# Performance work log

Measured on AMD Instinct MI355X. Metric: run time of the kernel, lower is better.

Reference implementation:

```python
import jax, jax.numpy as jnp
import numpy as np

B, S, M = 1, 2048, 2048
H, HKV, D = 32, 8, 64
SW = 128
WAVELENGTH = 150000.0
SCALE = D ** (-0.25)
NEG = -1e9  # large negative for fp32 compute dtype


def setup_inputs() -> dict:
    key = jax.random.key(0)
    ks = jax.random.split(key, 8)
    return {
        "hidden_states": jax.random.normal(ks[0], (B, S, M), jnp.float32),
        "Wq": jax.random.normal(ks[1], (M, H, D), jnp.float32) * 0.02,
        "bq": jnp.zeros((H, D), jnp.float32),
        "Wk": jax.random.normal(ks[2], (M, HKV, D), jnp.float32) * 0.02,
        "bk": jnp.zeros((HKV, D), jnp.float32),
        "Wv": jax.random.normal(ks[3], (M, HKV, D), jnp.float32) * 0.02,
        "bv": jnp.zeros((HKV, D), jnp.float32),
        "Wo": jax.random.normal(ks[4], (H, D, M), jnp.float32) * 0.02,
        "bo": jnp.zeros((M,), jnp.float32),
        "sinks": jax.random.normal(ks[5], (H,), jnp.float32),
    }


def _cos_sin(seq_len, dtype):
    # yarn RoPE with scaling_factor=1.0 reduces to standard RoPE (mscale=1,
    # no frequency interpolation). half = D//2 frequencies.
    half = D // 2
    inv_freq = 1.0 / (WAVELENGTH ** (jnp.arange(half, dtype=jnp.float32) * 2.0 / D))
    t = jnp.arange(seq_len, dtype=jnp.float32)
    freqs = t[:, None] * inv_freq[None, :]  # [S, half]
    # broadcast shape [1, S, 1, half] to match [B, S, heads, half]
    return (jnp.cos(freqs)[None, :, None, :].astype(dtype),
            jnp.sin(freqs)[None, :, None, :].astype(dtype))


def _interleaved_rope(x, cos, sin):
    x_even = x[..., ::2]
    x_odd = x[..., 1::2]
    first = x_even * cos - x_odd * sin
    second = x_odd * cos + x_even * sin
    return jnp.stack([first, second], axis=-1).reshape(x.shape)


def reference(hidden_states, Wq, bq, Wk, bk, Wv, bv, Wo, bo, sinks):
    b, s, _ = hidden_states.shape
    groups = H // HKV

    q = jnp.einsum('bqm,muh->bquh', hidden_states, Wq) + bq  # [B,S,H,D]
    k = jnp.einsum('bkm,mvh->bkvh', hidden_states, Wk) + bk  # [B,S,HKV,D]
    v = jnp.einsum('bkm,mvh->bkvh', hidden_states, Wv) + bv

    cos, sin = _cos_sin(s, hidden_states.dtype)
    q = _interleaved_rope(q, cos, sin) * SCALE
    k = _interleaved_rope(k, cos, sin) * SCALE

    # GQA: repeat kv heads to match query heads
    k = jnp.repeat(k, groups, axis=2)  # [B,S,H,D]
    v = jnp.repeat(v, groups, axis=2)

    scores = jnp.einsum('bquh,bkuh->buqk', q, k)  # [B,H,S,S]

    pos = jnp.arange(s)
    sw_mask = jnp.abs(pos[:, None] - pos[None, :]) <= SW  # bidirectional window
    scores = jnp.where(sw_mask[None, None, :, :], scores, NEG)

    sink_logits = jnp.broadcast_to(sinks[None, :, None, None], (b, H, s, 1))
    combined = jnp.concatenate([scores, sink_logits], axis=-1)  # [B,H,S,S+1]
    probs = jax.nn.softmax(combined.astype(jnp.float32), axis=-1)
    attn = probs[..., :-1].astype(hidden_states.dtype)  # drop sink column

    out = jnp.einsum('buqk,bkuh->bquh', attn, v)  # [B,S,H,D]
    return jnp.einsum('bquh,uhm->bqm', out, Wo) + bo
```

## Files before the change

kernel.cpp:

```cpp
#include <hip/hip_runtime.h>
#include <hip/hip_bf16.h>
#include <stdint.h>

typedef unsigned short u16;
typedef unsigned int   u32;

#define S_LEN 2048
#define NQKV  3072
#define NH    32
#define NKV   8
#define SWIN  128
#define NEGV  (-1.0e9f)
#define SCALE_Q 0.35355339059327379f

typedef __attribute__((ext_vector_type(4)))  float  f32x4;
typedef __attribute__((ext_vector_type(16))) float  f32x16;
typedef __attribute__((ext_vector_type(8)))  __bf16 bf16x8;

__device__ __forceinline__ u16 f2bf(float x){
  u32 u = __float_as_uint(x);
  return (u16)((u + 0x7fffu + ((u >> 16) & 1u)) >> 16);
}
__device__ __forceinline__ u32 pk2(float a, float b){
  return (u32)f2bf(a) | ((u32)f2bf(b) << 16);
}
__device__ __forceinline__ f32x4 mfma16(bf16x8 a, bf16x8 b, f32x4 c){
  return __builtin_amdgcn_mfma_f32_16x16x32_bf16(a, b, c, 0, 0, 0);
}
__device__ __forceinline__ f32x16 mfma32(bf16x8 a, bf16x8 b, f32x16 c){
  return __builtin_amdgcn_mfma_f32_32x32x16_bf16(a, b, c, 0, 0, 0);
}

typedef __attribute__((address_space(1))) const unsigned int ga_u32;
typedef __attribute__((address_space(3))) unsigned int       ls_u32;
__device__ __forceinline__ void gl16(const void* g, void* l){
  __builtin_amdgcn_global_load_lds((ga_u32*)g, (ls_u32*)l, 16, 0, 0);
}

__global__ __launch_bounds__(256) void k_prep(const float* __restrict__ bq,
                                              const float* __restrict__ bk,
                                              const float* __restrict__ bv,
                                              float* __restrict__ ropetab,
                                              float* __restrict__ bias3){
  int id = blockIdx.x * 256 + threadIdx.x;
  int t = id >> 5, i = id & 31;
  float e = (i * 2.0f) / 64.0f;
  float base = (float)pow(150000.0, (double)e);
  float invf = 1.0f / base;
  float fr = (float)t * invf;
  ropetab[(size_t)id * 2 + 0] = cosf(fr);
  ropetab[(size_t)id * 2 + 1] = sinf(fr);
  if (id < NQKV){
    float b;
    if (id < 2048) b = bq[id];
    else if (id < 2560) b = bk[id - 2048];
    else b = bv[id - 2560];
    bias3[id] = b;
  }
}

__device__ __forceinline__ void packw_seg(const float* __restrict__ w,
                                          u16* __restrict__ oh,
                                          int N, int NTot, int nOff, int id){
  int p = id / N, n = id % N;
  u32 hw[4];
  #pragma unroll
  for (int j = 0; j < 4; ++j){
    float a = w[(size_t)(8 * p + 2 * j) * N + n];
    float b = w[(size_t)(8 * p + 2 * j + 1) * N + n];
    hw[j] = pk2(a, b);
  }
  size_t o = ((size_t)p * NTot + nOff + n) * 8;
  *(uint4*)(oh + o) = make_uint4(hw[0], hw[1], hw[2], hw[3]);
}
__global__ __launch_bounds__(256) void k_packall(const float* __restrict__ hid,
                                                 const float* __restrict__ Wq,
                                                 const float* __restrict__ Wk,
                                                 const float* __restrict__ Wv,
                                                 const float* __restrict__ Wo,
                                                 u16* __restrict__ Ah,
                                                 u16* __restrict__ Bh,
                                                 u16* __restrict__ Woh){
  int b = blockIdx.x;
  if (b < 2048){
    int id = b * 256 + threadIdx.x;
    int r = id >> 8, p = id & 255;
    const float4* src = (const float4*)(hid + (size_t)id * 8);
    float4 v0 = src[0], v1 = src[1];
    u32 hw[4];
    hw[0] = pk2(v0.x, v0.y); hw[1] = pk2(v0.z, v0.w);
    hw[2] = pk2(v1.x, v1.y); hw[3] = pk2(v1.z, v1.w);
    int psw = (p & ~7) | ((p & 7) ^ (r & 7));
    size_t o = ((size_t)r * 256 + psw) * 8;
    *(uint4*)(Ah + o) = make_uint4(hw[0], hw[1], hw[2], hw[3]);
  } else if (b < 4096){
    packw_seg(Wq, Bh, 2048, NQKV, 0,    (b - 2048) * 256 + threadIdx.x);
  } else if (b < 4608){
    packw_seg(Wk, Bh, 512,  NQKV, 2048, (b - 4096) * 256 + threadIdx.x);
  } else if (b < 5120){
    packw_seg(Wv, Bh, 512,  NQKV, 2560, (b - 4608) * 256 + threadIdx.x);
  } else {
    packw_seg(Wo, Woh, 2048, 2048, 0,   (b - 5120) * 256 + threadIdx.x);
  }
}

template<bool ARM>
__global__ __launch_bounds__(256, 2) void k_gemm3(const u16* __restrict__ A,
                                                  const u16* __restrict__ B,
                                                  const float* __restrict__ bias,
                                                  float* __restrict__ C,
                                                  int M, int N, int K){
  __shared__ u16 lds[2][2][1024][8];
  const int tid = threadIdx.x;
  const int lane = tid & 63, wid = tid >> 6;
  const int q = lane & 15, g = lane >> 4;
  const int m0 = blockIdx.y * 128, n0 = blockIdx.x * 128;
  const int wr = wid >> 1, wc = wid & 1;
  const int pkK = K >> 3;

  f32x4 acc[4][4];
  #pragma unroll
  for (int a = 0; a < 4; ++a)
    #pragma unroll
    for (int b = 0; b < 4; ++b)
      #pragma unroll
      for (int r = 0; r < 4; ++r) acc[a][b][r] = 0.0f;

  size_t aoff[4], boff[4];
  #pragma unroll
  for (int c = 0; c < 4; ++c){
    int L = c * 256 + tid;
    if (ARM){
      int row = L >> 3, pa = L & 7;
      aoff[c] = ((size_t)(m0 + row) * pkK + pa) * 8;
    } else {
      int pa = L >> 7, row = L & 127;
      aoff[c] = ((size_t)pa * M + m0 + row) * 8;
    }
    int pb = L >> 7, col = L & 127;
    boff[c] = ((size_t)pb * N + n0 + col) * 8;
  }
  const size_t astep = ARM ? (size_t)64 : (size_t)64 * M;
  const size_t bstep = (size_t)64 * N;

  const int NT = K >> 6;

  auto STAGE = [&](int b){
    #pragma unroll
    for (int c = 0; c < 4; ++c){
      int lbase = c * 256 + wid * 64;
      gl16(A + aoff[c], &lds[b][0][lbase][0]);
      gl16(B + boff[c], &lds[b][1][lbase][0]);
      aoff[c] += astep; boff[c] += bstep;
    }
  };

  STAGE(0);
  STAGE(1);
  asm volatile("s_waitcnt vmcnt(8)" ::: "memory");
  __builtin_amdgcn_s_barrier();

  int buf = 0;
  for (int t = 0; t < NT; ++t){
    bf16x8 af[4][2], bf[4][2];
    #pragma unroll
    for (int ms = 0; ms < 4; ++ms){
      int row = wr * 64 + ms * 16 + q;
      #pragma unroll
      for (int kk = 0; kk < 2; ++kk){
        int ia = ARM ? (row * 8 + ((4 * kk + g) ^ (row & 7)))
                     : ((4 * kk + g) * 128 + row);
        af[ms][kk] = *(const bf16x8*)&lds[buf][0][ia][0];
      }
    }
    #pragma unroll
    for (int ns = 0; ns < 4; ++ns){
      int col = wc * 64 + ns * 16 + q;
      #pragma unroll
      for (int kk = 0; kk < 2; ++kk){
        int ib = (4 * kk + g) * 128 + col;
        bf[ns][kk] = *(const bf16x8*)&lds[buf][1][ib][0];
      }
    }
    asm volatile("s_waitcnt lgkmcnt(0)" ::: "memory");
    __builtin_amdgcn_sched_barrier(0);
    __builtin_amdgcn_s_barrier();
    if (t + 2 < NT) STAGE(buf);

    #pragma unroll
    for (int kk = 0; kk < 2; ++kk)
      #pragma unroll
      for (int ms = 0; ms < 4; ++ms)
        #pragma unroll
        for (int ns = 0; ns < 4; ++ns)
          acc[ms][ns] = mfma16(af[ms][kk], bf[ns][kk], acc[ms][ns]);

    if (t + 2 < NT){
      asm volatile("s_waitcnt vmcnt(8)" ::: "memory");
      __builtin_amdgcn_s_barrier();
    } else if (t + 1 < NT){
      asm volatile("s_waitcnt vmcnt(0)" ::: "memory");
      __builtin_amdgcn_s_barrier();
    }
    buf ^= 1;
  }

  #pragma unroll
  for (int ns = 0; ns < 4; ++ns){
    int col = n0 + wc * 64 + ns * 16 + q;
    float bb = bias[col];
    #pragma unroll
    for (int ms = 0; ms < 4; ++ms){
      int row = m0 + wr * 64 + ms * 16 + g * 4;
      #pragma unroll
      for (int r = 0; r < 4; ++r)
        C[(size_t)(row + r) * N + col] = acc[ms][ns][r] + bb;
    }
  }
}

__global__ __launch_bounds__(256) void k_rope(const float* __restrict__ qkv,
                                              const float* __restrict__ tab,
                                              u16* __restrict__ qoh,
                                              u16* __restrict__ koh){
  const int sL = threadIdx.x & 63, tp = threadIdx.x >> 6;
  const int s = blockIdx.x * 64 + sL;
  int h = blockIdx.y;
  u16* oh; int srcOff;
  if (h < NH){ oh = qoh; srcOff = h * 64; }
  else       { h -= NH; oh = koh; srcOff = 2048 + h * 64; }
  const float4* src = (const float4*)(qkv + (size_t)s * NQKV + srcOff + tp * 16);
  const float4* tb  = (const float4*)(tab + (size_t)s * 64 + tp * 16);
  float xv[16], tv[16];
  #pragma unroll
  for (int i = 0; i < 4; ++i){
    float4 a = src[i]; float4 b = tb[i];
    xv[4*i+0]=a.x; xv[4*i+1]=a.y; xv[4*i+2]=a.z; xv[4*i+3]=a.w;
    tv[4*i+0]=b.x; tv[4*i+1]=b.y; tv[4*i+2]=b.z; tv[4*i+3]=b.w;
  }
  u32 hw[8];
  #pragma unroll
  for (int j = 0; j < 8; ++j){
    float e = xv[2*j], o = xv[2*j+1];
    float c = tv[2*j], sn = tv[2*j+1];
    float f0 = (e * c - o * sn) * SCALE_Q;
    float f1 = (o * c + e * sn) * SCALE_Q;
    hw[j] = pk2(f0, f1);
  }
  size_t o0 = ((size_t)(h * 8 + tp * 2 + 0) * S_LEN + s) * 8;
  size_t o1 = ((size_t)(h * 8 + tp * 2 + 1) * S_LEN + s) * 8;
  *(uint4*)(oh + o0) = make_uint4(hw[0], hw[1], hw[2], hw[3]);
  *(uint4*)(oh + o1) = make_uint4(hw[4], hw[5], hw[6], hw[7]);
}

__global__ __launch_bounds__(256) void k_split_v2(const float* __restrict__ qkv,
                                                  u16* __restrict__ oh){
  __shared__ float tile[64][65];
  const int h = blockIdx.y;
  const int s0 = blockIdx.x * 64;
  {
    const int sL = threadIdx.x >> 2, ch = threadIdx.x & 3;
    const float4* rp = (const float4*)(qkv + (size_t)(s0 + sL) * NQKV + 2560 + h * 64 + ch * 16);
    #pragma unroll
    for (int i = 0; i < 4; ++i){
      float4 w = rp[i];
      tile[sL][ch * 16 + i * 4 + 0] = w.x;
      tile[sL][ch * 16 + i * 4 + 1] = w.y;
      tile[sL][ch * 16 + i * 4 + 2] = w.z;
      tile[sL][ch * 16 + i * 4 + 3] = w.w;
    }
  }
  __syncthreads();
  const int d = threadIdx.x & 63, spg = threadIdx.x >> 6;
  #pragma unroll
  for (int sp2 = 0; sp2 < 2; ++sp2){
    int spl = spg * 2 + sp2;
    float v[8];
    #pragma unroll
    for (int j = 0; j < 8; ++j) v[j] = tile[spl * 8 + j][d];
    u32 hw[4];
    #pragma unroll
    for (int j = 0; j < 4; ++j) hw[j] = pk2(v[2*j], v[2*j+1]);
    size_t o_ = (((size_t)h * 256 + blockIdx.x * 8 + spl) * 64 + d) * 8;
    *(uint4*)(oh + o_) = make_uint4(hw[0], hw[1], hw[2], hw[3]);
  }
}

__global__ __launch_bounds__(256) void k_attn(const u16* __restrict__ qh,
                                              const u16* __restrict__ kh,
                                              const u16* __restrict__ vh,
                                              const float* __restrict__ sinks,
                                              u16* __restrict__ aoh){
  const int lane = threadIdx.x & 63;
  const int wid = threadIdx.x >> 6;
  const int h = blockIdx.x;
  const int hkv = h >> 2;
  const int q0 = blockIdx.y * 128 + wid * 32;
  const int lq = lane & 31;
  const int half = lane >> 5;
  const int qi = q0 + lq;

  bf16x8 qf[4];
  #pragma unroll
  for (int st = 0; st < 4; ++st){
    size_t off = (((size_t)h * 8 + st * 2 + half) * S_LEN + qi) * 8;
    qf[st] = *(const bf16x8*)(qh + off);
  }
  float m = sinks[h];
  float lsum = 1.0f;
  f32x16 o0, o1;
  #pragma unroll
  for (int r = 0; r < 16; ++r){ o0[r] = 0.0f; o1[r] = 0.0f; }

  const int kb0 = q0 - 128;
  for (int c = 0; c < 9; ++c){
    const int kb = kb0 + c * 32;
    if (kb + 32 <= 0 || kb >= S_LEN) continue;
    const int keyr = kb + lq;
    const int keyc = min(max(keyr, 0), S_LEN - 1);
    f32x16 sc;
    #pragma unroll
    for (int r = 0; r < 16; ++r) sc[r] = 0.0f;
    #pragma unroll
    for (int st = 0; st < 4; ++st){
      size_t ko = (((size_t)hkv * 8 + st * 2 + half) * S_LEN + keyc) * 8;
      bf16x8 kf = *(const bf16x8*)(kh + ko);
      sc = mfma32(kf, qf[st], sc);
    }
    float tmax = -3.0e38f;
    #pragma unroll
    for (int r = 0; r < 16; ++r){
      int key = kb + (r & 3) + 8 * (r >> 2) + 4 * half;
      int dd = qi - key; if (dd < 0) dd = -dd;
      bool ok = (key >= 0) && (key < S_LEN) && (dd <= SWIN);
      sc[r] = ok ? sc[r] : NEGV;
      tmax = fmaxf(tmax, sc[r]);
    }
    tmax = fmaxf(tmax, __shfl_xor(tmax, 32));
    float mn = fmaxf(m, tmax);
    float alpha = __expf(m - mn);
    m = mn;
    float p[16]; float ps = 0.0f;
    #pragma unroll
    for (int r = 0; r < 16; ++r){ p[r] = __expf(sc[r] - mn); ps += p[r]; }
    ps += __shfl_xor(ps, 32);
    lsum = lsum * alpha + ps;
    #pragma unroll
    for (int r = 0; r < 16; ++r){ o0[r] *= alpha; o1[r] *= alpha; }
    u32 wh[8];
    #pragma unroll
    for (int j = 0; j < 8; ++j) wh[j] = pk2(p[2 * j], p[2 * j + 1]);
    bf16x8 pfh[2];
    #pragma unroll
    for (int ks = 0; ks < 2; ++ks){
      u32 x0 = wh[4 * ks + 0], y0 = wh[4 * ks + 2];
      u32 x1 = wh[4 * ks + 1], y1 = wh[4 * ks + 3];
      u32 sx0 = __shfl_xor(x0, 32), sy0 = __shfl_xor(y0, 32);
      u32 sx1 = __shfl_xor(x1, 32), sy1 = __shfl_xor(y1, 32);
      union { u32 u[4]; bf16x8 b; } fb;
      fb.u[0] = half ? sy0 : x0;
      fb.u[1] = half ? sy1 : x1;
      fb.u[2] = half ? y0 : sx0;
      fb.u[3] = half ? y1 : sx1;
      pfh[ks] = fb.b;
    }
    #pragma unroll
    for (int ks = 0; ks < 2; ++ks){
      int kp = kb / 8 + ks * 2 + half;
      kp = min(max(kp, 0), S_LEN / 8 - 1);
      #pragma unroll
      for (int nt = 0; nt < 2; ++nt){
        size_t vo = (((size_t)hkv * 256 + kp) * 64 + nt * 32 + lq) * 8;
        bf16x8 vf = *(const bf16x8*)(vh + vo);
        f32x16 acc = (nt == 0) ? o0 : o1;
        acc = mfma32(vf, pfh[ks], acc);
        if (nt == 0) o0 = acc; else o1 = acc;
      }
    }
  }
  float inv = 1.0f / lsum;
  #pragma unroll
  for (int nt = 0; nt < 2; ++nt){
    f32x16 o = (nt == 0) ? o0 : o1;
    #pragma unroll
    for (int rr = 0; rr < 4; ++rr){
      int d0 = nt * 32 + 8 * rr + 4 * half;
      float v0 = o[rr * 4 + 0] * inv, v1 = o[rr * 4 + 1] * inv;
      float v2 = o[rr * 4 + 2] * inv, v3 = o[rr * 4 + 3] * inv;
      int kp_ = h * 8 + nt * 4 + rr;
      size_t oo = ((size_t)kp_ * S_LEN + qi) * 8 + (d0 & 7);
      uint2 wv; wv.x = pk2(v0, v1); wv.y = pk2(v2, v3);
      *(uint2*)(aoh + oo) = wv;
    }
  }
}

extern "C" void kernel_launch(void* const* d_in, const int* in_sizes, int n_in,
                              void* d_out, int out_size, void* d_ws, size_t ws_size,
                              hipStream_t stream){
  const float* hid = (const float*)d_in[0];
  const float* Wq  = (const float*)d_in[1];
  const float* bq  = (const float*)d_in[2];
  const float* Wk  = (const float*)d_in[3];
  const float* bk  = (const float*)d_in[4];
  const float* Wv  = (const float*)d_in[5];
  const float* bv  = (const float*)d_in[6];
  const float* Wo  = (const float*)d_in[7];
  const float* bo  = (const float*)d_in[8];
  const float* sinks = (const float*)d_in[9];
  float* out = (float*)d_out;

  char* w = (char*)d_ws;
  size_t off = 0;
  auto alloc = [&](size_t bytes){ void* p = w + off; off += (bytes + 255) & ~(size_t)255; return p; };
  float* ropetab = (float*)alloc((size_t)S_LEN * 32 * 2 * 4);
  float* bias3   = (float*)alloc((size_t)NQKV * 4);
  u16* Ah  = (u16*)alloc((size_t)2048 * 2048 * 2);
  u16* Bh  = (u16*)alloc((size_t)256 * NQKV * 8 * 2);
  float* QKV = (float*)alloc((size_t)S_LEN * NQKV * 4);
  u16* qph = (u16*)alloc((size_t)NH * 8 * S_LEN * 8 * 2);
  u16* kph = (u16*)alloc((size_t)NKV * 8 * S_LEN * 8 * 2);
  u16* vph = (u16*)alloc((size_t)NKV * 256 * 64 * 8 * 2);
  u16* aoh = (u16*)alloc((size_t)256 * S_LEN * 8 * 2);
  u16* Woh = (u16*)alloc((size_t)256 * 2048 * 8 * 2);
  (void)in_sizes; (void)n_in; (void)out_size; (void)ws_size;

  k_prep<<<256, 256, 0, stream>>>(bq, bk, bv, ropetab, bias3);
  k_packall<<<7168, 256, 0, stream>>>(hid, Wq, Wk, Wv, Wo, Ah, Bh, Woh);
  k_gemm3<true><<<dim3(NQKV / 128, 2048 / 128), 256, 0, stream>>>(Ah, Bh, bias3, QKV,
                                                                  2048, NQKV, 2048);
  k_rope<<<dim3(32, NH + NKV), 256, 0, stream>>>(QKV, ropetab, qph, kph);
  k_split_v2<<<dim3(32, NKV), 256, 0, stream>>>(QKV, vph);
  k_attn<<<dim3(NH, S_LEN / 128), 256, 0, stream>>>(qph, kph, vph, sinks, aoh);
  k_gemm3<false><<<dim3(2048 / 128, 2048 / 128), 256, 0, stream>>>(aoh, Woh, bo, out,
                                                                   2048, 2048, 2048);
}
```

Baseline: 201.8 us.

## Fuse RoPE and V repacking into QKV GEMM epilogue

The QKV projection GEMM now applies RoPE, scaling and bf16 packing directly in its epilogue. It writes Q/K/V straight into the attention-ready layouts instead of first storing an fp32 QKV buffer. This removes the intermediate buffer's write and read traffic and two kernel launches. The cost is narrow 2-byte scattered stores and lane shuffles in the epilogue, which may coalesce poorly.

```diff
diff --git a/kernel.cpp b/kernel.cpp
--- a/kernel.cpp
+++ b/kernel.cpp
@@ -104,10 +104,14 @@
   }
 }
 
-template<bool ARM>
+template<bool ARM, int EPI>
 __global__ __launch_bounds__(256, 2) void k_gemm3(const u16* __restrict__ A,
                                                   const u16* __restrict__ B,
                                                   const float* __restrict__ bias,
+                                                  const float* __restrict__ tab,
+                                                  u16* __restrict__ qoh,
+                                                  u16* __restrict__ koh,
+                                                  u16* __restrict__ voh,
                                                   float* __restrict__ C,
                                                   int M, int N, int K){
   __shared__ u16 lds[2][2][1024][8];
@@ -205,84 +209,54 @@
     buf ^= 1;
   }
 
-  #pragma unroll
-  for (int ns = 0; ns < 4; ++ns){
-    int col = n0 + wc * 64 + ns * 16 + q;
-    float bb = bias[col];
-    #pragma unroll
-    for (int ms = 0; ms < 4; ++ms){
-      int row = m0 + wr * 64 + ms * 16 + g * 4;
-      #pragma unroll
-      for (int r = 0; r < 4; ++r)
-        C[(size_t)(row + r) * N + col] = acc[ms][ns][r] + bb;
-    }
-  }
-}
-
-__global__ __launch_bounds__(256) void k_rope(const float* __restrict__ qkv,
-                                              const float* __restrict__ tab,
-                                              u16* __restrict__ qoh,
-                                              u16* __restrict__ koh){
-  const int sL = threadIdx.x & 63, tp = threadIdx.x >> 6;
-  const int s = blockIdx.x * 64 + sL;
-  int h = blockIdx.y;
-  u16* oh; int srcOff;
-  if (h < NH){ oh = qoh; srcOff = h * 64; }
-  else       { h -= NH; oh = koh; srcOff = 2048 + h * 64; }
-  const float4* src = (const float4*)(qkv + (size_t)s * NQKV + srcOff + tp * 16);
-  const float4* tb  = (const float4*)(tab + (size_t)s * 64 + tp * 16);
-  float xv[16], tv[16];
-  #pragma unroll
-  for (int i = 0; i < 4; ++i){
-    float4 a = src[i]; float4 b = tb[i];
-    xv[4*i+0]=a.x; xv[4*i+1]=a.y; xv[4*i+2]=a.z; xv[4*i+3]=a.w;
-    tv[4*i+0]=b.x; tv[4*i+1]=b.y; tv[4*i+2]=b.z; tv[4*i+3]=b.w;
-  }
-  u32 hw[8];
-  #pragma unroll
-  for (int j = 0; j < 8; ++j){
-    float e = xv[2*j], o = xv[2*j+1];
-    float c = tv[2*j], sn = tv[2*j+1];
-    float f0 = (e * c - o * sn) * SCALE_Q;
-    float f1 = (o * c + e * sn) * SCALE_Q;
-    hw[j] = pk2(f0, f1);
-  }
-  size_t o0 = ((size_t)(h * 8 + tp * 2 + 0) * S_LEN + s) * 8;
-  size_t o1 = ((size_t)(h * 8 + tp * 2 + 1) * S_LEN + s) * 8;
-  *(uint4*)(oh + o0) = make_uint4(hw[0], hw[1], hw[2], hw[3]);
-  *(uint4*)(oh + o1) = make_uint4(hw[4], hw[5], hw[6], hw[7]);
-}
-
-__global__ __launch_bounds__(256) void k_split_v2(const float* __restrict__ qkv,
-                                                  u16* __restrict__ oh){
-  __shared__ float tile[64][65];
-  const int h = blockIdx.y;
-  const int s0 = blockIdx.x * 64;
-  {
-    const int sL = threadIdx.x >> 2, ch = threadIdx.x & 3;
-    const float4* rp = (const float4*)(qkv + (size_t)(s0 + sL) * NQKV + 2560 + h * 64 + ch * 16);
-    #pragma unroll
-    for (int i = 0; i < 4; ++i){
-      float4 w = rp[i];
-      tile[sL][ch * 16 + i * 4 + 0] = w.x;
-      tile[sL][ch * 16 + i * 4 + 1] = w.y;
-      tile[sL][ch * 16 + i * 4 + 2] = w.z;
-      tile[sL][ch * 16 + i * 4 + 3] = w.w;
-    }
-  }
-  __syncthreads();
-  const int d = threadIdx.x & 63, spg = threadIdx.x >> 6;
-  #pragma unroll
-  for (int sp2 = 0; sp2 < 2; ++sp2){
-    int spl = spg * 2 + sp2;
-    float v[8];
-    #pragma unroll
-    for (int j = 0; j < 8; ++j) v[j] = tile[spl * 8 + j][d];
-    u32 hw[4];
-    #pragma unroll
-    for (int j = 0; j < 4; ++j) hw[j] = pk2(v[2*j], v[2*j+1]);
-    size_t o_ = (((size_t)h * 256 + blockIdx.x * 8 + spl) * 64 + d) * 8;
-    *(uint4*)(oh + o_) = make_uint4(hw[0], hw[1], hw[2], hw[3]);
+  if (EPI == 0){
+    #pragma unroll
+    for (int ns = 0; ns < 4; ++ns){
+      int col = n0 + wc * 64 + ns * 16 + q;
+      float bb = bias[col];
+      #pragma unroll
+      for (int ms = 0; ms < 4; ++ms){
+        int row = m0 + wr * 64 + ms * 16 + g * 4;
+        #pragma unroll
+        for (int r = 0; r < 4; ++r)
+          C[(size_t)(row + r) * N + col] = acc[ms][ns][r] + bb;
+      }
+    }
+  } else {
+    const int ttype = (n0 < 2048) ? 0 : (n0 < 2560 ? 1 : 2);
+    const bool ev = (q & 1) == 0;
+    #pragma unroll
+    for (int ns = 0; ns < 4; ++ns){
+      int col = n0 + wc * 64 + ns * 16 + q;
+      float bb = bias[col];
+      int j = (col & 63) >> 1;
+      #pragma unroll
+      for (int ms = 0; ms < 4; ++ms){
+        int rbase = m0 + wr * 64 + ms * 16 + g * 4;
+        #pragma unroll
+        for (int r = 0; r < 4; ++r){
+          int row = rbase + r;
+          float val = acc[ms][ns][r] + bb;
+          if (ttype < 2){
+            float pr = __shfl_xor(val, 1);
+            float e = ev ? val : pr, o = ev ? pr : val;
+            float2 cs = *(const float2*)(tab + ((size_t)row * 32 + j) * 2);
+            float outv = (ev ? (e * cs.x - o * cs.y)
+                             : (o * cs.x + e * cs.y)) * SCALE_Q;
+            if (ttype == 0){
+              int h = col >> 6, pk = (col & 63) >> 3;
+              qoh[(((size_t)(h * 8 + pk)) * S_LEN + row) * 8 + (col & 7)] = f2bf(outv);
+            } else {
+              int h = (col - 2048) >> 6, pk = (col & 63) >> 3;
+              koh[(((size_t)(h * 8 + pk)) * S_LEN + row) * 8 + (col & 7)] = f2bf(outv);
+            }
+          } else {
+            int hv = (col - 2560) >> 6, d = col & 63;
+            voh[(((size_t)(hv * 256 + (row >> 3))) * 64 + d) * 8 + (row & 7)] = f2bf(val);
+          }
+        }
+      }
+    }
   }
 }
 
@@ -417,7 +391,6 @@
   float* bias3   = (float*)alloc((size_t)NQKV * 4);
   u16* Ah  = (u16*)alloc((size_t)2048 * 2048 * 2);
   u16* Bh  = (u16*)alloc((size_t)256 * NQKV * 8 * 2);
-  float* QKV = (float*)alloc((size_t)S_LEN * NQKV * 4);
   u16* qph = (u16*)alloc((size_t)NH * 8 * S_LEN * 8 * 2);
   u16* kph = (u16*)alloc((size_t)NKV * 8 * S_LEN * 8 * 2);
   u16* vph = (u16*)alloc((size_t)NKV * 256 * 64 * 8 * 2);
@@ -427,11 +400,9 @@
 
   k_prep<<<256, 256, 0, stream>>>(bq, bk, bv, ropetab, bias3);
   k_packall<<<7168, 256, 0, stream>>>(hid, Wq, Wk, Wv, Wo, Ah, Bh, Woh);
-  k_gemm3<true><<<dim3(NQKV / 128, 2048 / 128), 256, 0, stream>>>(Ah, Bh, bias3, QKV,
-                                                                  2048, NQKV, 2048);
-  k_rope<<<dim3(32, NH + NKV), 256, 0, stream>>>(QKV, ropetab, qph, kph);
-  k_split_v2<<<dim3(32, NKV), 256, 0, stream>>>(QKV, vph);
+  k_gemm3<true, 1><<<dim3(NQKV / 128, 2048 / 128), 256, 0, stream>>>(
+      Ah, Bh, bias3, ropetab, qph, kph, vph, nullptr, 2048, NQKV, 2048);
   k_attn<<<dim3(NH, S_LEN / 128), 256, 0, stream>>>(qph, kph, vph, sinks, aoh);
-  k_gemm3<false><<<dim3(2048 / 128, 2048 / 128), 256, 0, stream>>>(aoh, Woh, bo, out,
-                                                                   2048, 2048, 2048);
-}
+  k_gemm3<false, 0><<<dim3(2048 / 128, 2048 / 128), 256, 0, stream>>>(
+      aoh, Woh, bo, nullptr, nullptr, nullptr, nullptr, out, 2048, 2048, 2048);
+}
```

Result: slower. 208.7 us (+3.4%).
